# Kernel optimization log

Measured on AMD Instinct MI355X. Metric: run time of the kernel, lower is better.

The kernel has to match this reference:

```python
import jax, jax.numpy as jnp
import numpy as np

NUM_NODES = 1_000_000
EMBED_DIM = 64
HIDDEN_DIM = 128


def setup_inputs() -> dict:
    key = jax.random.key(0)
    k_e, k_emb, k_w1, k_b1, k_w2, k_b2 = jax.random.split(key, 6)
    edge_index = jax.random.randint(k_e, (2, 1_250_000), 0, NUM_NODES, dtype=jnp.int64)
    emb = jax.random.normal(k_emb, (NUM_NODES, EMBED_DIM), dtype=jnp.float32)
    # torch.nn.Linear: y = x @ W.T + b ; store W as [out, in] to match
    w1 = jax.random.normal(k_w1, (HIDDEN_DIM, EMBED_DIM), dtype=jnp.float32) * (1.0 / np.sqrt(EMBED_DIM))
    b1 = jax.random.normal(k_b1, (HIDDEN_DIM,), dtype=jnp.float32) * 0.01
    w2 = jax.random.normal(k_w2, (EMBED_DIM, HIDDEN_DIM), dtype=jnp.float32) * (1.0 / np.sqrt(HIDDEN_DIM))
    b2 = jax.random.normal(k_b2, (EMBED_DIM,), dtype=jnp.float32) * 0.01
    return {"edge_index": edge_index, "emb": emb, "w1": w1, "b1": b1, "w2": w2, "b2": b2}


def reference(edge_index, emb, w1, b1, w2, b2):
    src, dst = edge_index[0], edge_index[1]
    # scatter-add: messages[dst] += emb[src]  (vectorized over all edges)
    messages = jnp.zeros_like(emb).at[dst].add(emb[src])  # [N, D]
    aggregated = jax.nn.relu(messages @ w1.T + b1)         # [N, H]
    updated = jax.nn.relu(aggregated @ w2.T + b2)          # [N, D]
    return emb + updated
```

## Files before the change

### kernel.cpp

```cpp
#include <hip/hip_runtime.h>

#define N_NODES 1000000
#define D 64
#define H 128

typedef float f4 __attribute__((ext_vector_type(4)));

__global__ __launch_bounds__(256) void detect_kernel(const unsigned int* __restrict__ e,
                                                     int* __restrict__ flag) {
    __shared__ int any_nz;
    if (threadIdx.x == 0) any_nz = 0;
    __syncthreads();
    int nz = 0;
    for (int k = threadIdx.x; k < 2048; k += 256) {
        if (e[2 * k + 1] != 0u) nz = 1;
    }
    if (nz) atomicOr(&any_nz, 1);
    __syncthreads();
    if (threadIdx.x == 0) *flag = any_nz;
}

__global__ __launch_bounds__(256) void transpose_w2_kernel(const float* __restrict__ w2,
                                                           float* __restrict__ w2t) {
    int idx = blockIdx.x * 256 + threadIdx.x;
    if (idx < D * H) {
        int i = idx >> 7;
        int j = idx & (H - 1);
        w2t[j * D + i] = w2[idx];
    }
}

__global__ __launch_bounds__(256) void scatter_kernel(const void* __restrict__ edges,
                                                      const float* __restrict__ emb,
                                                      float* __restrict__ msg,
                                                      const int* __restrict__ flag,
                                                      int E) {
    int idx  = blockIdx.x * 256 + threadIdx.x;
    int e    = idx >> 6;
    int lane = idx & 63;
    if (e >= E) return;

    long long s, d;
    if (*flag) {
        const int* p = (const int*)edges;
        s = p[e];
        d = p[E + e];
    } else {
        const long long* p = (const long long*)edges;
        s = p[e];
        d = p[E + e];
    }

    float v = emb[s * (long long)D + lane];
    atomicAdd(msg + d * (long long)D + lane, v);
}

__global__ __launch_bounds__(256)
__attribute__((amdgpu_waves_per_eu(2, 3)))
void mlp_kernel(float* __restrict__ io,
                const float* __restrict__ emb,
                const float* __restrict__ w1,
                const float* __restrict__ b1,
                const float* __restrict__ w2t,
                const float* __restrict__ b2) {
    int n = blockIdx.x * 256 + threadIdx.x;
    if (n >= N_NODES) return;

    const f4* __restrict__ mp = (const f4*)(io + (size_t)n * D);
    f4 m[D / 4];
#pragma unroll
    for (int c = 0; c < D / 4; ++c) m[c] = mp[c];

    const f4* __restrict__ b2v = (const f4*)b2;
    f4 u[D / 4];
#pragma unroll
    for (int c = 0; c < D / 4; ++c) u[c] = b2v[c];

#pragma unroll 2
    for (int j = 0; j < H; ++j) {
        const f4* __restrict__ wr = (const f4*)(w1 + j * D);
        f4 acc = (f4){0.0f, 0.0f, 0.0f, 0.0f};
#pragma unroll
        for (int c = 0; c < D / 4; ++c) acc = m[c] * wr[c] + acc;
        float h = (acc[0] + acc[1]) + (acc[2] + acc[3]) + b1[j];
        h = fmaxf(h, 0.0f);

        const f4* __restrict__ wc = (const f4*)(w2t + j * D);
#pragma unroll
        for (int c = 0; c < D / 4; ++c) u[c] = h * wc[c] + u[c];
    }

    const f4* __restrict__ ev = (const f4*)(emb + (size_t)n * D);
    f4* __restrict__ ov = (f4*)(io + (size_t)n * D);
#pragma unroll
    for (int c = 0; c < D / 4; ++c) {
        f4 r;
        r[0] = ev[c][0] + fmaxf(u[c][0], 0.0f);
        r[1] = ev[c][1] + fmaxf(u[c][1], 0.0f);
        r[2] = ev[c][2] + fmaxf(u[c][2], 0.0f);
        r[3] = ev[c][3] + fmaxf(u[c][3], 0.0f);
        ov[c] = r;
    }
}

extern "C" void kernel_launch(void* const* d_in, const int* in_sizes, int n_in,
                              void* d_out, int out_size, void* d_ws, size_t ws_size,
                              hipStream_t stream) {
    const void*  edges = d_in[0];
    const float* emb   = (const float*)d_in[1];
    const float* w1    = (const float*)d_in[2];
    const float* b1    = (const float*)d_in[3];
    const float* w2    = (const float*)d_in[4];
    const float* b2    = (const float*)d_in[5];
    float*       out   = (float*)d_out;

    int*   flag = (int*)d_ws;
    float* w2t  = (float*)((char*)d_ws + 256);

    const int E = in_sizes[0] / 2;

    hipMemsetAsync(out, 0, (size_t)N_NODES * D * sizeof(float), stream);

    detect_kernel<<<1, 256, 0, stream>>>((const unsigned int*)edges, flag);
    transpose_w2_kernel<<<(D * H + 255) / 256, 256, 0, stream>>>(w2, w2t);

    long long sthreads = (long long)E * 64;
    int       sblocks  = (int)((sthreads + 255) / 256);
    scatter_kernel<<<sblocks, 256, 0, stream>>>(edges, emb, out, flag, E);

    int mblocks = (N_NODES + 255) / 256;
    mlp_kernel<<<mblocks, 256, 0, stream>>>(out, emb, w1, b1, w2t, b2);
}
```

Baseline: 1.308 ms.

## Split MLP into fp16 hidden kernel and half-width output kernel, use packed atomics

The fused MLP kernel is split into two kernels. The first computes the hidden layer and stores it in place as fp16, 128 halves fitting the 64-float row. The second assigns two waves per node, each producing half of the output columns, so it needs fewer live registers and can run at higher occupancy. The scatter now uses packed 2-float atomic adds, halving the thread and atomic count. The trade-offs are an extra round trip through global memory for the hidden activations and reduced precision from storing them in fp16.

```diff
diff --git a/kernel.cpp b/kernel.cpp
--- a/kernel.cpp
+++ b/kernel.cpp
@@ -5,6 +5,8 @@
 #define H 128
 
 typedef float f4 __attribute__((ext_vector_type(4)));
+typedef float v2f __attribute__((ext_vector_type(2)));
+typedef _Float16 h8 __attribute__((ext_vector_type(8)));
 
 __global__ __launch_bounds__(256) void detect_kernel(const unsigned int* __restrict__ e,
                                                      int* __restrict__ flag) {
@@ -35,9 +37,9 @@
                                                       float* __restrict__ msg,
                                                       const int* __restrict__ flag,
                                                       int E) {
-    int idx  = blockIdx.x * 256 + threadIdx.x;
-    int e    = idx >> 6;
-    int lane = idx & 63;
+    long long t = (long long)blockIdx.x * 256 + threadIdx.x;
+    int e  = (int)(t >> 5);
+    int pr = (int)(t & 31);
     if (e >= E) return;
 
     long long s, d;
@@ -51,18 +53,23 @@
         d = p[E + e];
     }
 
-    float v = emb[s * (long long)D + lane];
-    atomicAdd(msg + d * (long long)D + lane, v);
+    v2f v = *((const v2f*)(emb + s * (long long)D) + pr);
+    float* dp = msg + d * (long long)D + pr * 2;
+
+#if __has_builtin(__builtin_amdgcn_global_atomic_fadd_v2f32)
+    typedef v2f __attribute__((address_space(1)))* gv2f;
+    __builtin_amdgcn_global_atomic_fadd_v2f32((gv2f)(v2f*)dp, v);
+#else
+    atomicAdd(dp, v[0]);
+    atomicAdd(dp + 1, v[1]);
+#endif
 }
 
 __global__ __launch_bounds__(256)
-__attribute__((amdgpu_waves_per_eu(2, 3)))
-void mlp_kernel(float* __restrict__ io,
-                const float* __restrict__ emb,
-                const float* __restrict__ w1,
-                const float* __restrict__ b1,
-                const float* __restrict__ w2t,
-                const float* __restrict__ b2) {
+__attribute__((amdgpu_waves_per_eu(5, 5)))
+void hidden_kernel(float* __restrict__ io,
+                   const float* __restrict__ w1,
+                   const float* __restrict__ b1) {
     int n = blockIdx.x * 256 + threadIdx.x;
     if (n >= N_NODES) return;
 
@@ -71,35 +78,72 @@
 #pragma unroll
     for (int c = 0; c < D / 4; ++c) m[c] = mp[c];
 
-    const f4* __restrict__ b2v = (const f4*)b2;
-    f4 u[D / 4];
-#pragma unroll
-    for (int c = 0; c < D / 4; ++c) u[c] = b2v[c];
+    h8* __restrict__ hp = (h8*)(io + (size_t)n * D);
 
 #pragma unroll 2
-    for (int j = 0; j < H; ++j) {
-        const f4* __restrict__ wr = (const f4*)(w1 + j * D);
-        f4 acc = (f4){0.0f, 0.0f, 0.0f, 0.0f};
+    for (int jb = 0; jb < H / 8; ++jb) {
+        h8 hv;
 #pragma unroll
-        for (int c = 0; c < D / 4; ++c) acc = m[c] * wr[c] + acc;
-        float h = (acc[0] + acc[1]) + (acc[2] + acc[3]) + b1[j];
-        h = fmaxf(h, 0.0f);
+        for (int t = 0; t < 8; ++t) {
+            int j = jb * 8 + t;
+            const f4* __restrict__ wr = (const f4*)(w1 + j * D);
+            f4 acc = (f4){0.0f, 0.0f, 0.0f, 0.0f};
+#pragma unroll
+            for (int c = 0; c < D / 4; ++c) acc = m[c] * wr[c] + acc;
+            float h = (acc[0] + acc[1]) + (acc[2] + acc[3]) + b1[j];
+            hv[t] = (_Float16)fmaxf(h, 0.0f);
+        }
+        hp[jb] = hv;
+    }
+}
 
-        const f4* __restrict__ wc = (const f4*)(w2t + j * D);
+__global__ __launch_bounds__(256) void out_kernel(float* __restrict__ io,
+                                                  const float* __restrict__ emb,
+                                                  const float* __restrict__ w2t,
+                                                  const float* __restrict__ b2) {
+    int tid  = blockIdx.x * 256 + threadIdx.x;
+    int wave = tid >> 6;
+    int lane = tid & 63;
+    int half = wave & 1;
+    int n    = (wave >> 1) * 64 + lane;
+    bool active = (n < N_NODES);
+
+    f4 u[8];
+
+    if (active) {
+        const f4* __restrict__ b2v = (const f4*)(b2 + half * 32);
 #pragma unroll
-        for (int c = 0; c < D / 4; ++c) u[c] = h * wc[c] + u[c];
+        for (int c = 0; c < 8; ++c) u[c] = b2v[c];
+
+        const h8* __restrict__ hp = (const h8*)(io + (size_t)n * D);
+#pragma unroll 2
+        for (int jb = 0; jb < H / 8; ++jb) {
+            h8 hv = hp[jb];
+#pragma unroll
+            for (int t = 0; t < 8; ++t) {
+                float h = (float)hv[t];
+                const f4* __restrict__ wc =
+                    (const f4*)(w2t + (jb * 8 + t) * D + half * 32);
+#pragma unroll
+                for (int c = 0; c < 8; ++c) u[c] = h * wc[c] + u[c];
+            }
+        }
     }
 
-    const f4* __restrict__ ev = (const f4*)(emb + (size_t)n * D);
-    f4* __restrict__ ov = (f4*)(io + (size_t)n * D);
+    __syncthreads();
+
+    if (active) {
+        const f4* __restrict__ ev = (const f4*)(emb + (size_t)n * D + half * 32);
+        f4* __restrict__ ov = (f4*)(io + (size_t)n * D + half * 32);
 #pragma unroll
-    for (int c = 0; c < D / 4; ++c) {
-        f4 r;
-        r[0] = ev[c][0] + fmaxf(u[c][0], 0.0f);
-        r[1] = ev[c][1] + fmaxf(u[c][1], 0.0f);
-        r[2] = ev[c][2] + fmaxf(u[c][2], 0.0f);
-        r[3] = ev[c][3] + fmaxf(u[c][3], 0.0f);
-        ov[c] = r;
+        for (int c = 0; c < 8; ++c) {
+            f4 r;
+            r[0] = ev[c][0] + fmaxf(u[c][0], 0.0f);
+            r[1] = ev[c][1] + fmaxf(u[c][1], 0.0f);
+            r[2] = ev[c][2] + fmaxf(u[c][2], 0.0f);
+            r[3] = ev[c][3] + fmaxf(u[c][3], 0.0f);
+            ov[c] = r;
+        }
     }
 }
 
@@ -124,10 +168,13 @@
     detect_kernel<<<1, 256, 0, stream>>>((const unsigned int*)edges, flag);
     transpose_w2_kernel<<<(D * H + 255) / 256, 256, 0, stream>>>(w2, w2t);
 
-    long long sthreads = (long long)E * 64;
+    long long sthreads = (long long)E * 32;
     int       sblocks  = (int)((sthreads + 255) / 256);
     scatter_kernel<<<sblocks, 256, 0, stream>>>(edges, emb, out, flag, E);
 
-    int mblocks = (N_NODES + 255) / 256;
-    mlp_kernel<<<mblocks, 256, 0, stream>>>(out, emb, w1, b1, w2t, b2);
+    int hblocks = (N_NODES + 255) / 256;
+    hidden_kernel<<<hblocks, 256, 0, stream>>>(out, w1, b1);
+
+    int oblocks = (N_NODES * 2 + 255) / 256;
+    out_kernel<<<oblocks, 256, 0, stream>>>(out, emb, w2t, b2);
 }
```

New measurement: 2.486 ms. +90.1%, slower.
